# Optimization experiments

Hardware: AMD Instinct MI355X
Metric: run time of the kernel (lower is better)

The kernel has to match this reference:

```python
import jax, jax.numpy as jnp
import numpy as np

B, S, D = 4, 4096, 1024
H, HID, ATT = 16, 64, 64


def setup_inputs() -> dict:
    key = jax.random.key(0)
    ks = jax.random.split(key, 7)
    sc = 0.02
    return {
        "x": jax.random.normal(ks[0], (B, S, D), dtype=jnp.float32),
        "Wq": jax.random.normal(ks[1], (D, H * HID), dtype=jnp.float32) * sc,
        "bq": jnp.zeros((H * HID,), dtype=jnp.float32),
        "Wk": jax.random.normal(ks[2], (D, H * HID), dtype=jnp.float32) * sc,
        "bk": jnp.zeros((H * HID,), dtype=jnp.float32),
        "Wv": jax.random.normal(ks[3], (D, H * ATT), dtype=jnp.float32) * sc,
        "bv": jnp.zeros((H * ATT,), dtype=jnp.float32),
    }


def reference(x, Wq, bq, Wk, bk, Wv, bv):
    b, s, _ = x.shape
    q = (x @ Wq + bq).reshape(b, s, H, HID)
    k = (x @ Wk + bk).reshape(b, s, H, HID)
    v = (x @ Wv + bv).reshape(b, s, H, ATT)
    # attention across the head axis: [B,S,H,H] scores per token
    scores = jnp.einsum("bsid,bsjd->bsij", q, k) / np.sqrt(HID).astype(np.float32)
    probs = jax.nn.softmax(scores, axis=-1)
    ctx = jnp.einsum("bsij,bsja->bsia", probs, v)
    return ctx.reshape(b, s, H * ATT)
```

## Files before the change

### kernel.cpp

```cpp
#include <hip/hip_runtime.h>


#define AS1 __attribute__((address_space(1)))
#define AS3 __attribute__((address_space(3)))

typedef __bf16 bf16x8 __attribute__((ext_vector_type(8)));
typedef float f32x4 __attribute__((ext_vector_type(4)));
typedef float f32x16 __attribute__((ext_vector_type(16)));
typedef unsigned short u16x8 __attribute__((ext_vector_type(8)));

static constexpr int MTOK = 16384;
static constexpr int N3   = 3072;
static constexpr int KD   = 1024;

__device__ __forceinline__ unsigned short f2bf(float f) {
  unsigned u = __float_as_uint(f);
  unsigned r = u + 0x7FFFu + ((u >> 16) & 1u);
  return (unsigned short)(r >> 16);
}
__device__ __forceinline__ float bf2f(unsigned short s) {
  return __uint_as_float(((unsigned)s) << 16);
}

__device__ __forceinline__ void gload_lds16(const void* g, void* lds_ptr) {
  __builtin_amdgcn_global_load_lds((const AS1 void*)g, (AS3 void*)lds_ptr, 16, 0, 0);
}

__global__ __launch_bounds__(256) void cvt_x_kernel(const float* __restrict__ x,
                                                    unsigned short* __restrict__ xb) {
  int i = blockIdx.x * 256 + threadIdx.x;
  const float4* p = (const float4*)x;
  float4 a = p[2 * i], b = p[2 * i + 1];
  u16x8 o;
  o[0] = f2bf(a.x); o[1] = f2bf(a.y); o[2] = f2bf(a.z); o[3] = f2bf(a.w);
  o[4] = f2bf(b.x); o[5] = f2bf(b.y); o[6] = f2bf(b.z); o[7] = f2bf(b.w);
  *((u16x8*)xb + i) = o;
}

__global__ __launch_bounds__(256) void prep_w_kernel(const float* __restrict__ Wq,
                                                     const float* __restrict__ Wk,
                                                     const float* __restrict__ Wv,
                                                     const float* __restrict__ bq,
                                                     const float* __restrict__ bk,
                                                     const float* __restrict__ bv,
                                                     unsigned short* __restrict__ WT,
                                                     float* __restrict__ bcat) {
  __shared__ float tile[32][33];
  int kt = blockIdx.x * 32;
  int nt = blockIdx.y * 32;
  const float* W; const float* bias; int nb;
  if (nt < 1024)      { W = Wq; bias = bq; nb = nt; }
  else if (nt < 2048) { W = Wk; bias = bk; nb = nt - 1024; }
  else                { W = Wv; bias = bv; nb = nt - 2048; }
  int tx = threadIdx.x & 31, ty = threadIdx.x >> 5;
#pragma unroll
  for (int it = 0; it < 4; ++it) {
    int kk = it * 8 + ty;
    tile[kk][tx] = W[(size_t)(kt + kk) * 1024 + nb + tx];
  }
  __syncthreads();
#pragma unroll
  for (int it = 0; it < 4; ++it) {
    int nn = it * 8 + ty;
    WT[(size_t)(nt + nn) * 1024 + kt + tx] = f2bf(tile[tx][nn]);
  }
  if (blockIdx.x == 0 && threadIdx.x < 32)
    bcat[nt + threadIdx.x] = bias[nb + threadIdx.x];
}

__global__ __launch_bounds__(512, 2) void gemm_qkv_kernel(const unsigned short* __restrict__ A,
                                                          const unsigned short* __restrict__ Bt,
                                                          const float* __restrict__ bias,
                                                          unsigned short* __restrict__ C) {
  __shared__ __align__(16) unsigned short lds[65536];
  const int tid  = threadIdx.x;
  const int lane = tid & 63;
  const int wave = tid >> 6;
  const int wm = wave >> 2, wn = wave & 3;
  const int m0 = blockIdx.x * 256;
  const int n0 = blockIdx.y * 256;

  const size_t afrow = (size_t)(m0 + wave * 32 + (lane & 31)) * KD + ((lane >> 5) * 8);
  const size_t bfrow = (size_t)(n0 + wave * 32 + (lane & 31)) * KD + ((lane >> 5) * 8);
  const int dbase = wave * 1024 + lane * 8;

  int aoff[4][2], boff[2][2];
#pragma unroll
  for (int m = 0; m < 4; ++m)
#pragma unroll
    for (int ks = 0; ks < 2; ++ks)
      aoff[m][ks] = ((wm * 4 + m) * 2 + ks) * 512 + lane * 8;
#pragma unroll
  for (int n = 0; n < 2; ++n)
#pragma unroll
    for (int ks = 0; ks < 2; ++ks)
      boff[n][ks] = 8192 + ((wn * 2 + n) * 2 + ks) * 512 + lane * 8;

  f32x16 acc[4][2] = {};

#define STAGE(SLOT, KK)                                                        \
  do {                                                                         \
    unsigned short* da = lds + (SLOT) * 16384 + dbase;                         \
    gload_lds16(A  + afrow + (KK),      da);                                   \
    gload_lds16(A  + afrow + (KK) + 16, da + 512);                             \
    gload_lds16(Bt + bfrow + (KK),      da + 8192);                            \
    gload_lds16(Bt + bfrow + (KK) + 16, da + 8704);                            \
  } while (0)

#define PH(SLOT, DOSTAGE, KSTG)                                                \
  do {                                                                         \
    const unsigned short* bufp = lds + (SLOT) * 16384;                         \
    bf16x8 af[4][2], bfr[2][2];                                                \
    _Pragma("unroll") for (int m = 0; m < 4; ++m)                              \
      _Pragma("unroll") for (int ks = 0; ks < 2; ++ks)                         \
        af[m][ks] = *(const bf16x8*)(bufp + aoff[m][ks]);                      \
    _Pragma("unroll") for (int n = 0; n < 2; ++n)                              \
      _Pragma("unroll") for (int ks = 0; ks < 2; ++ks)                         \
        bfr[n][ks] = *(const bf16x8*)(bufp + boff[n][ks]);                     \
    if (DOSTAGE) { STAGE(((SLOT) + 3) & 3, KSTG); }                            \
    __builtin_amdgcn_s_setprio(1);                                             \
    _Pragma("unroll") for (int ks = 0; ks < 2; ++ks)                           \
      _Pragma("unroll") for (int m = 0; m < 4; ++m)                            \
        _Pragma("unroll") for (int n = 0; n < 2; ++n)                          \
          acc[m][n] = __builtin_amdgcn_mfma_f32_32x32x16_bf16(af[m][ks],       \
                          bfr[n][ks], acc[m][n], 0, 0, 0);                     \
    __builtin_amdgcn_s_setprio(0);                                             \
  } while (0)

#define SYNC(VM)                                                               \
  do {                                                                         \
    asm volatile("s_waitcnt vmcnt(" #VM ")" ::: "memory");                     \
    __builtin_amdgcn_s_barrier();                                              \
  } while (0)

  STAGE(0, 0); STAGE(1, 32); STAGE(2, 64);

#pragma unroll 1
  for (int t = 0; t < 7; ++t) {
    const int kb = t * 128;
    SYNC(8); PH(0, true, kb + 96);
    SYNC(8); PH(1, true, kb + 128);
    SYNC(8); PH(2, true, kb + 160);
    SYNC(8); PH(3, true, kb + 192);
  }
  SYNC(8); PH(0, true, 992);
  SYNC(8); PH(1, false, 0);
  SYNC(4); PH(2, false, 0);
  SYNC(0); PH(3, false, 0);
#undef STAGE
#undef PH
#undef SYNC

#pragma unroll
  for (int n = 0; n < 2; ++n) {
    int col = n0 + wn * 64 + n * 32 + (lane & 31);
    float bvv = bias[col];
#pragma unroll
    for (int m = 0; m < 4; ++m) {
      int rowb = m0 + wm * 128 + m * 32 + 4 * (lane >> 5);
#pragma unroll
      for (int r = 0; r < 16; ++r) {
        int row = rowb + (r & 3) + 8 * (r >> 2);
        C[(size_t)row * N3 + col] = f2bf(acc[m][n][r] + bvv);
      }
    }
  }
}

__global__ __launch_bounds__(256) void attn_kernel(const unsigned short* __restrict__ qkv,
                                                   float* __restrict__ out) {
  __shared__ float p_lds[4][16][17];
  const int tid = threadIdx.x;
  const int lane = tid & 63;
  const int w = tid >> 6;
  const size_t token = (size_t)blockIdx.x * 4 + w;
  const unsigned short* rowp = qkv + token * N3;
  const int head = lane & 15;
  const int chunk = lane >> 4;

  const int o = head * 64 + chunk * 8;
  bf16x8 q0 = *(const bf16x8*)(rowp + o);
  bf16x8 q1 = *(const bf16x8*)(rowp + o + 32);
  bf16x8 k0 = *(const bf16x8*)(rowp + 1024 + o);
  bf16x8 k1 = *(const bf16x8*)(rowp + 1024 + o + 32);
  f32x4 c = {0.f, 0.f, 0.f, 0.f};
  c = __builtin_amdgcn_mfma_f32_16x16x32_bf16(q0, k0, c, 0, 0, 0);
  c = __builtin_amdgcn_mfma_f32_16x16x32_bf16(q1, k1, c, 0, 0, 0);

#pragma unroll
  for (int r = 0; r < 4; ++r) {
    float s = c[r] * 0.125f;
    float m = s;
#pragma unroll
    for (int off = 1; off < 16; off <<= 1) m = fmaxf(m, __shfl_xor(m, off, 64));
    float e = __expf(s - m);
    float sum = e;
#pragma unroll
    for (int off = 1; off < 16; off <<= 1) sum += __shfl_xor(sum, off, 64);
    p_lds[w][chunk * 4 + r][head] = e / sum;
  }
  __syncthreads();

  const int i = lane >> 2;
  const int ab = lane & 3;
  const unsigned short* vbase = rowp + 2048 + ab * 16;
  float accv[16];
#pragma unroll
  for (int cc = 0; cc < 16; ++cc) accv[cc] = 0.f;
#pragma unroll
  for (int j = 0; j < 16; ++j) {
    float pij = p_lds[w][i][j];
    u16x8 v0 = *(const u16x8*)(vbase + j * 64);
    u16x8 v1 = *(const u16x8*)(vbase + j * 64 + 8);
#pragma unroll
    for (int cc = 0; cc < 8; ++cc) accv[cc] += pij * bf2f(v0[cc]);
#pragma unroll
    for (int cc = 0; cc < 8; ++cc) accv[8 + cc] += pij * bf2f(v1[cc]);
  }
  float* op = out + token * 1024 + i * 64 + ab * 16;
#pragma unroll
  for (int cc = 0; cc < 16; cc += 4) {
    f32x4 v = {accv[cc], accv[cc + 1], accv[cc + 2], accv[cc + 3]};
    *(f32x4*)(op + cc) = v;
  }
}

extern "C" void kernel_launch(void* const* d_in, const int* in_sizes, int n_in,
                              void* d_out, int out_size, void* d_ws, size_t ws_size,
                              hipStream_t stream) {
  const float* x  = (const float*)d_in[0];
  const float* Wq = (const float*)d_in[1];
  const float* bq = (const float*)d_in[2];
  const float* Wk = (const float*)d_in[3];
  const float* bk = (const float*)d_in[4];
  const float* Wv = (const float*)d_in[5];
  const float* bv = (const float*)d_in[6];
  float* out = (float*)d_out;

  char* ws = (char*)d_ws;
  unsigned short* xb   = (unsigned short*)ws;
  unsigned short* WT   = (unsigned short*)(ws + 33554432);
  float*          bcat = (float*)(ws + 39845888);
  unsigned short* qkv  = (unsigned short*)(ws + 39858176);

  cvt_x_kernel<<<dim3((MTOK * KD / 8) / 256), 256, 0, stream>>>(x, xb);
  prep_w_kernel<<<dim3(32, 96), 256, 0, stream>>>(Wq, Wk, Wv, bq, bk, bv, WT, bcat);
  gemm_qkv_kernel<<<dim3(MTOK / 256, N3 / 256), 512, 0, stream>>>(xb, WT, bcat, qkv);
  attn_kernel<<<dim3(MTOK / 4), 256, 0, stream>>>(qkv, out);
}
```

Before: 181.1 us.

## Load A fragments directly to registers and stage only B through LDS

The QKV GEMM now gives each wave its own 64-row A slice, read straight from global memory into registers and double-buffered one k-step ahead. Only the shared B tile still goes through the 4-slot LDS ring, so LDS use is halved. The wave layout changes from 2x4 to 4x2 (64x128 per wave) and a sched_barrier pins the ordering of loads and MFMAs. This is meant to cut LDS traffic and footprint, at the cost of more register pressure and A rows that are no longer shared across waves through LDS, which can expose global-load latency.

```diff
diff --git a/kernel.cpp b/kernel.cpp
--- a/kernel.cpp
+++ b/kernel.cpp
@@ -72,57 +72,59 @@
                                                           const unsigned short* __restrict__ Bt,
                                                           const float* __restrict__ bias,
                                                           unsigned short* __restrict__ C) {
-  __shared__ __align__(16) unsigned short lds[65536];
+  __shared__ __align__(16) unsigned short lds[32768];
   const int tid  = threadIdx.x;
   const int lane = tid & 63;
   const int wave = tid >> 6;
-  const int wm = wave >> 2, wn = wave & 3;
+  const int wm = wave >> 1, wn = wave & 1;
   const int m0 = blockIdx.x * 256;
   const int n0 = blockIdx.y * 256;
 
-  const size_t afrow = (size_t)(m0 + wave * 32 + (lane & 31)) * KD + ((lane >> 5) * 8);
-  const size_t bfrow = (size_t)(n0 + wave * 32 + (lane & 31)) * KD + ((lane >> 5) * 8);
-  const int dbase = wave * 1024 + lane * 8;
-
-  int aoff[4][2], boff[2][2];
-#pragma unroll
-  for (int m = 0; m < 4; ++m)
+  const unsigned short* Ap = A + (size_t)(m0 + wm * 64 + (lane & 31)) * KD + ((lane >> 5) * 8);
+
+  const size_t bsrc0 = (size_t)(n0 + (wave >> 1) * 32 + (lane & 31)) * KD
+                       + (wave & 1) * 16 + ((lane >> 5) * 8);
+  const size_t bsrc1 = bsrc0 + (size_t)128 * KD;
+
+  int boff[4][2];
+#pragma unroll
+  for (int n = 0; n < 4; ++n)
 #pragma unroll
     for (int ks = 0; ks < 2; ++ks)
-      aoff[m][ks] = ((wm * 4 + m) * 2 + ks) * 512 + lane * 8;
-#pragma unroll
-  for (int n = 0; n < 2; ++n)
-#pragma unroll
-    for (int ks = 0; ks < 2; ++ks)
-      boff[n][ks] = 8192 + ((wn * 2 + n) * 2 + ks) * 512 + lane * 8;
-
-  f32x16 acc[4][2] = {};
-
-#define STAGE(SLOT, KK)                                                        \
-  do {                                                                         \
-    unsigned short* da = lds + (SLOT) * 16384 + dbase;                         \
-    gload_lds16(A  + afrow + (KK),      da);                                   \
-    gload_lds16(A  + afrow + (KK) + 16, da + 512);                             \
-    gload_lds16(Bt + bfrow + (KK),      da + 8192);                            \
-    gload_lds16(Bt + bfrow + (KK) + 16, da + 8704);                            \
-  } while (0)
-
-#define PH(SLOT, DOSTAGE, KSTG)                                                \
-  do {                                                                         \
-    const unsigned short* bufp = lds + (SLOT) * 16384;                         \
-    bf16x8 af[4][2], bfr[2][2];                                                \
-    _Pragma("unroll") for (int m = 0; m < 4; ++m)                              \
+      boff[n][ks] = ((wn * 4 + n) * 2 + ks) * 512 + lane * 8;
+
+  f32x16 acc[2][4] = {};
+  bf16x8 aP[2][2], aQ[2][2];
+
+#define STAGE_B(SLOT, KK)                                                      \
+  do {                                                                         \
+    unsigned short* d0 = lds + (SLOT) * 8192 + tid * 8;                        \
+    gload_lds16(Bt + bsrc0 + (KK), d0);                                        \
+    gload_lds16(Bt + bsrc1 + (KK), d0 + 4096);                                 \
+  } while (0)
+
+#define LOAD_A(DST, KK)                                                        \
+  do {                                                                         \
+    _Pragma("unroll") for (int m = 0; m < 2; ++m)                              \
       _Pragma("unroll") for (int ks = 0; ks < 2; ++ks)                         \
-        af[m][ks] = *(const bf16x8*)(bufp + aoff[m][ks]);                      \
-    _Pragma("unroll") for (int n = 0; n < 2; ++n)                              \
+        DST[m][ks] = *(const bf16x8*)(Ap + (size_t)m * 32 * KD + (KK) + ks * 16);\
+  } while (0)
+
+#define BODY(SLOT, AC, AN, KSL, DOSTAGE, DOLOADA)                              \
+  do {                                                                         \
+    const unsigned short* bufp = lds + (SLOT) * 8192;                          \
+    bf16x8 bfr[4][2];                                                          \
+    _Pragma("unroll") for (int n = 0; n < 4; ++n)                              \
       _Pragma("unroll") for (int ks = 0; ks < 2; ++ks)                         \
         bfr[n][ks] = *(const bf16x8*)(bufp + boff[n][ks]);                     \
-    if (DOSTAGE) { STAGE(((SLOT) + 3) & 3, KSTG); }                            \
+    if (DOLOADA) { LOAD_A(AN, (KSL) + 32); }                                   \
+    if (DOSTAGE) { STAGE_B(((SLOT) + 3) & 3, (KSL) + 96); }                    \
+    __builtin_amdgcn_sched_barrier(0);                                         \
     __builtin_amdgcn_s_setprio(1);                                             \
     _Pragma("unroll") for (int ks = 0; ks < 2; ++ks)                           \
-      _Pragma("unroll") for (int m = 0; m < 4; ++m)                            \
-        _Pragma("unroll") for (int n = 0; n < 2; ++n)                          \
-          acc[m][n] = __builtin_amdgcn_mfma_f32_32x32x16_bf16(af[m][ks],       \
+      _Pragma("unroll") for (int m = 0; m < 2; ++m)                            \
+        _Pragma("unroll") for (int n = 0; n < 4; ++n)                          \
+          acc[m][n] = __builtin_amdgcn_mfma_f32_32x32x16_bf16(AC[m][ks],       \
                           bfr[n][ks], acc[m][n], 0, 0, 0);                     \
     __builtin_amdgcn_s_setprio(0);                                             \
   } while (0)
@@ -133,31 +135,34 @@
     __builtin_amdgcn_s_barrier();                                              \
   } while (0)
 
-  STAGE(0, 0); STAGE(1, 32); STAGE(2, 64);
+  LOAD_A(aP, 0);
+  STAGE_B(0, 0); STAGE_B(1, 32); STAGE_B(2, 64);
+  SYNC(4);
 
 #pragma unroll 1
   for (int t = 0; t < 7; ++t) {
     const int kb = t * 128;
-    SYNC(8); PH(0, true, kb + 96);
-    SYNC(8); PH(1, true, kb + 128);
-    SYNC(8); PH(2, true, kb + 160);
-    SYNC(8); PH(3, true, kb + 192);
-  }
-  SYNC(8); PH(0, true, 992);
-  SYNC(8); PH(1, false, 0);
-  SYNC(4); PH(2, false, 0);
-  SYNC(0); PH(3, false, 0);
-#undef STAGE
-#undef PH
+    BODY(0, aP, aQ, kb,       true, true); SYNC(8);
+    BODY(1, aQ, aP, kb + 32,  true, true); SYNC(8);
+    BODY(2, aP, aQ, kb + 64,  true, true); SYNC(8);
+    BODY(3, aQ, aP, kb + 96,  true, true); SYNC(8);
+  }
+  BODY(0, aP, aQ, 896, true,  true);  SYNC(8);
+  BODY(1, aQ, aP, 928, false, true);  SYNC(6);
+  BODY(2, aP, aQ, 960, false, true);  SYNC(4);
+  BODY(3, aQ, aP, 992, false, false);
+#undef STAGE_B
+#undef LOAD_A
+#undef BODY
 #undef SYNC
 
 #pragma unroll
-  for (int n = 0; n < 2; ++n) {
-    int col = n0 + wn * 64 + n * 32 + (lane & 31);
+  for (int n = 0; n < 4; ++n) {
+    int col = n0 + wn * 128 + n * 32 + (lane & 31);
     float bvv = bias[col];
 #pragma unroll
-    for (int m = 0; m < 4; ++m) {
-      int rowb = m0 + wm * 128 + m * 32 + 4 * (lane >> 5);
+    for (int m = 0; m < 2; ++m) {
+      int rowb = m0 + wm * 64 + m * 32 + 4 * (lane >> 5);
 #pragma unroll
       for (int r = 0; r < 16; ++r) {
         int row = rowb + (r & 3) + 8 * (r >> 2);
```

After: 236.4 us. 1.31x slower.
